# Optimization experiments

Measured on AMD Instinct MI355X. Metric: run time of the kernel, lower is better.

The kernel has to match this reference:

```python
import jax, jax.numpy as jnp
import numpy as np


def _ln(x, w, b, eps=1e-5):
    m = x.mean(-1, keepdims=True)
    v = jnp.mean((x - m) ** 2, axis=-1, keepdims=True)
    return (x - m) * jax.lax.rsqrt(v + eps) * w + b


def _to_seq(xc, g):
    # xc: [B,Di,H,W] -> [B,L,Di]; g0: row-major fwd, g1: row-major rev,
    # g2: col-major fwd, g3: col-major rev (CrossScan_1..4)
    if g >= 2:
        xc = xc.transpose(0, 1, 3, 2)
    s = xc.reshape(xc.shape[0], xc.shape[1], -1)
    if g % 2 == 1:
        s = jnp.flip(s, -1)
    return s.transpose(0, 2, 1)


def _from_seq(y, g, H, W):
    # y: [B,L,Di] -> [B,H,W,Di], inverse of _to_seq (CrossMerge_1..4)
    if g % 2 == 1:
        y = jnp.flip(y, 1)
    Bn, L, Di = y.shape
    if g >= 2:
        return y.reshape(Bn, W, H, Di).transpose(0, 2, 1, 3)
    return y.reshape(Bn, H, W, Di)


def _sscan(dA, dBx, Cm):
    # selective scan: h_t = dA_t*h + dBx_t ; y_t = <h_t, C_t>
    # dA,dBx: [B,L,Di,S], Cm: [B,L,S] -> y: [B,L,Di]
    def step(h, inp):
        a, bx, c = inp
        h = a * h + bx
        return h, jnp.einsum('bds,bs->bd', h, c)
    h0 = jnp.zeros(dA.shape[:1] + dA.shape[2:], dA.dtype)
    _, ys = jax.lax.scan(step, h0, (dA.transpose(1, 0, 2, 3), dBx.transpose(1, 0, 2, 3), Cm.transpose(1, 0, 2)))
    return ys.transpose(1, 0, 2)


def _ss2d(xc, g, H, W, ipw, ipb, cw, cb, xpw, dtw, dtb, A_log, Ds, onw, onb, opw, opb):
    R = dtw.shape[-1]
    S = A_log.shape[-1]
    xz = xc @ ipw.T + ipb                      # [B,H,W,2*Di]
    Di = xz.shape[-1] // 2
    xi, z = xz[..., :Di], xz[..., Di:]
    xi = xi.transpose(0, 3, 1, 2)              # [B,Di,H,W]
    xi = jax.lax.conv_general_dilated(xi, cw, (1, 1), [(1, 1), (1, 1)],
                                      dimension_numbers=('NCHW', 'OIHW', 'NCHW'),
                                      feature_group_count=Di) + cb[None, :, None, None]
    xi = jax.nn.silu(xi)
    seq = _to_seq(xi, g)                       # [B,L,Di]
    xdbl = seq @ xpw.T                         # [B,L,R+2S]
    dtr, Bm, Cm = xdbl[..., :R], xdbl[..., R:R + S], xdbl[..., R + S:]
    dt = jax.nn.softplus(dtr @ dtw.T + dtb)    # [B,L,Di]
    A = -jnp.exp(A_log)                        # [Di,S]
    dA = jnp.exp(dt[..., None] * A)            # [B,L,Di,S]
    dBx = (dt * seq)[..., None] * Bm[:, :, None, :]
    y = _sscan(dA, dBx, Cm) + Ds * seq
    y = _from_seq(y, g, H, W)                  # [B,H,W,Di]
    y = _ln(y, onw, onb)
    y = y * jax.nn.silu(z)
    return y @ opw.T + opb


def setup_inputs() -> dict:
    Bn, Hh, Ww, C = 8, 96, 96, 256
    Di = C // 4
    S = 1
    R = max(1, (Di + 15) // 16)
    key = jax.random.key(0)
    ks = jax.random.split(key, 12)
    nrm = lambda k, sh, s: jax.random.normal(k, sh, jnp.float32) * s
    return {
        'x': nrm(ks[0], (Bn, Hh * Ww, C), 1.0),
        'norm_w': jnp.ones((C,), jnp.float32), 'norm_b': jnp.zeros((C,), jnp.float32),
        'fc_w': nrm(ks[1], (C, C), 0.02), 'fc_b': jnp.zeros((C,), jnp.float32),
        'conv1d_w': nrm(ks[2], (1, 1, 3), 0.3),
        'in_proj_w': nrm(ks[3], (4, 2 * Di, Di), 0.05), 'in_proj_b': jnp.zeros((4, 2 * Di), jnp.float32),
        'conv2d_w': nrm(ks[4], (4, Di, 1, 3, 3), 0.2), 'conv2d_b': jnp.zeros((4, Di), jnp.float32),
        'x_proj_w': nrm(ks[5], (4, R + 2 * S, Di), 0.05),
        'dt_w': nrm(ks[6], (4, Di, R), 0.1), 'dt_b': nrm(ks[7], (4, Di), 0.1),
        'A_log': nrm(ks[8], (4, Di, S), 0.1),
        'Ds': jnp.ones((4, Di), jnp.float32),
        'out_norm_w': jnp.ones((4, Di), jnp.float32), 'out_norm_b': jnp.zeros((4, Di), jnp.float32),
        'out_proj_w': nrm(ks[9], (4, Di, Di), 0.05), 'out_proj_b': jnp.zeros((4, Di), jnp.float32),
        'proj_w': nrm(ks[10], (C, C), 0.02), 'proj_b': jnp.zeros((C,), jnp.float32),
        'skip_scale': jnp.ones((1,), jnp.float32),
        'H': Hh, 'W': Ww,
    }


def reference(x, norm_w, norm_b, fc_w, fc_b, conv1d_w, in_proj_w, in_proj_b, conv2d_w, conv2d_b,
              x_proj_w, dt_w, dt_b, A_log, Ds, out_norm_w, out_norm_b, out_proj_w, out_proj_b,
              proj_w, proj_b, skip_scale, H, W):
    B, N, C = x.shape
    xn = _ln(x, norm_w, norm_b)
    z_avg = xn.mean(1)                         # [B,C] (permute(0,2,1).mean(2))
    yg = jax.lax.conv_general_dilated(z_avg[:, None, :], conv1d_w, (1,), [(1, 1)],
                                      dimension_numbers=('NCH', 'OIH', 'NCH'))[:, 0, :]
    gate = jax.nn.sigmoid(z_avg @ fc_w.T + fc_b + yg)   # fc_out_2 [B,C]
    xg = xn.reshape(B, H, W, C)
    Dg = C // 4
    outs = [_ss2d(xg[..., g * Dg:(g + 1) * Dg], g, H, W,
                  in_proj_w[g], in_proj_b[g], conv2d_w[g], conv2d_b[g], x_proj_w[g],
                  dt_w[g], dt_b[g], A_log[g], Ds[g], out_norm_w[g], out_norm_b[g],
                  out_proj_w[g], out_proj_b[g]) for g in range(4)]
    xm = jnp.concatenate(outs, -1) * skip_scale * xg
    xm = xm.reshape(B, N, C) * gate[:, None, :]
    xm = _ln(xm, norm_w, norm_b)
    return xm @ proj_w.T + proj_b
```

## Files before the change

### kernel.cpp

```cpp
#include <hip/hip_runtime.h>
#include <math.h>

#define HH 96
#define WWI 96
#define NN 9216
#define CC 256
#define LL 9216
#define CHK 96
#define NCH 96
#define BB 8
#define BN (BB*NN)

__device__ __forceinline__ float softplusf(float x){
    float e = expf(-fabsf(x));
    return fmaxf(x, 0.f) + log1pf(e);
}
__device__ __forceinline__ float sigmf(float x){ return 1.f / (1.f + expf(-x)); }

__device__ __forceinline__ float wredsum(float v){
    #pragma unroll
    for(int o = 32; o > 0; o >>= 1) v += __shfl_xor(v, o, 64);
    return v;
}

__device__ __forceinline__ void wredsum2(float& s, float& q){
    #pragma unroll
    for(int o = 32; o > 0; o >>= 1){
        s += __shfl_xor(s, o, 64);
        q += __shfl_xor(q, o, 64);
    }
}

__device__ __forceinline__ void chunk_walk(int g, int chunk, int& base, int& step){
    if(g == 0){ base = chunk * 96;        step = 1;   }
    else if(g == 1){ base = 9215 - chunk * 96; step = -1; }
    else if(g == 2){ base = chunk;        step = 96;  }
    else { base = 9215 - chunk;           step = -96; }
}

__global__ __launch_bounds__(256) void k_stats(const float* __restrict__ x,
                                               float* __restrict__ mrs){
    int wid = threadIdx.x >> 6, lane = threadIdx.x & 63;
    size_t row = (size_t)blockIdx.x * 4 + wid;
    float4 v = ((const float4*)(x + row * CC))[lane];
    float s = wredsum(v.x + v.y + v.z + v.w);
    float q = wredsum(v.x*v.x + v.y*v.y + v.z*v.z + v.w*v.w);
    float m = s * (1.f/256.f);
    float var = q * (1.f/256.f) - m*m;
    float rs = rsqrtf(fmaxf(var, 0.f) + 1e-5f);
    if(lane == 0){ mrs[2*row] = m; mrs[2*row+1] = rs; }
}

__global__ __launch_bounds__(256) void k_prew(const float* __restrict__ pw,
        const float* __restrict__ nw, const float* __restrict__ nb,
        const float* __restrict__ pb, float* __restrict__ Wn,
        float* __restrict__ wsum, float* __restrict__ cvec){
    int o = threadIdx.x;
    float ws = 0.f, cc = 0.f;
    for(int k = 0; k < 256; k++){
        float w = pw[(size_t)o * 256 + k];
        float wn = w * nw[k];
        Wn[(size_t)o * 256 + k] = wn;
        ws += wn; cc += w * nb[k];
    }
    wsum[o] = ws; cvec[o] = cc + pb[o];
}

__global__ __launch_bounds__(256) void k_zavg(const float* __restrict__ x,
        const float* __restrict__ mrs, const float* __restrict__ nw,
        const float* __restrict__ nb, float* __restrict__ zpart){
    int c = threadIdx.x, b = blockIdx.y, t0 = blockIdx.x * 256;
    float nwv = nw[c], nbv = nb[c];
    float s = 0.f;
    for(int i = 0; i < 256; i++){
        size_t r = (size_t)b * NN + t0 + i;
        s += (x[r * CC + c] - mrs[2*r]) * mrs[2*r+1] * nwv + nbv;
    }
    zpart[((size_t)b * 36 + blockIdx.x) * CC + c] = s;
}

__global__ __launch_bounds__(256) void k_gate(const float* __restrict__ zpart,
        const float* __restrict__ fcw, const float* __restrict__ fcb,
        const float* __restrict__ w1d, float* __restrict__ gate){
    __shared__ float za[CC];
    int c = threadIdx.x, b = blockIdx.x;
    float s = 0.f;
    for(int t = 0; t < 36; t++) s += zpart[((size_t)b * 36 + t) * CC + c];
    za[c] = s * (1.f/(float)NN);
    __syncthreads();
    float zm1 = (c > 0)     ? za[c-1] : 0.f;
    float zp1 = (c < CC-1)  ? za[c+1] : 0.f;
    float acc = fcb[c] + w1d[0]*zm1 + w1d[1]*za[c] + w1d[2]*zp1;
    const float* wr = fcw + (size_t)c * CC;
    for(int k = 0; k < CC; k++) acc += za[k] * wr[k];
    gate[b * CC + c] = sigmf(acc);
}

__global__ __launch_bounds__(256) void k_inproj(const float* __restrict__ x,
        const float* __restrict__ mrs, const float* __restrict__ nw,
        const float* __restrict__ nb, const float* __restrict__ ipw,
        const float* __restrict__ ipb, float* __restrict__ xib,
        float* __restrict__ zbuf){
    int tile = blockIdx.x, b = blockIdx.y, g = blockIdx.z;
    int n0 = tile * 128;
    __shared__ float xs[128 * 64];
    int tid = threadIdx.x;
    for(int idx = tid; idx < 2048; idx += 256){
        int p = idx >> 4, k4 = (idx & 15) * 4;
        size_t r = (size_t)b * NN + n0 + p;
        float4 v = *(const float4*)(x + r * CC + g*64 + k4);
        float m = mrs[2*r], rs = mrs[2*r+1];
        float4 w4 = *(const float4*)(nw + g*64 + k4);
        float4 b4 = *(const float4*)(nb + g*64 + k4);
        float4 o;
        o.x = (v.x - m)*rs*w4.x + b4.x;
        o.y = (v.y - m)*rs*w4.y + b4.y;
        o.z = (v.z - m)*rs*w4.z + b4.z;
        o.w = (v.w - m)*rs*w4.w + b4.w;
        *(float4*)(xs + p*64 + k4) = o;
    }
    __syncthreads();
    int c = tid & 63, ph = tid >> 6;
    float wx[64], wz[64];
    {
        const float* wrx = ipw + ((size_t)(g*128 + c)) * 64;
        const float* wrz = ipw + ((size_t)(g*128 + 64 + c)) * 64;
        #pragma unroll
        for(int k = 0; k < 64; k++){ wx[k] = wrx[k]; wz[k] = wrz[k]; }
    }
    float bx = ipb[g*128 + c], bz = ipb[g*128 + 64 + c];
    size_t obase = ((size_t)(b*4 + g)) * NN + n0;
    for(int p = ph*32; p < ph*32 + 32; p++){
        const float4* xp = (const float4*)(xs + p*64);
        float a0 = 0.f, a1 = 0.f, z0 = 0.f, z1 = 0.f;
        #pragma unroll
        for(int k4 = 0; k4 < 16; k4 += 2){
            float4 u = xp[k4], v = xp[k4+1];
            a0 += u.x*wx[4*k4+0]; a1 += u.y*wx[4*k4+1];
            a0 += u.z*wx[4*k4+2]; a1 += u.w*wx[4*k4+3];
            z0 += u.x*wz[4*k4+0]; z1 += u.y*wz[4*k4+1];
            z0 += u.z*wz[4*k4+2]; z1 += u.w*wz[4*k4+3];
            a0 += v.x*wx[4*k4+4]; a1 += v.y*wx[4*k4+5];
            a0 += v.z*wx[4*k4+6]; a1 += v.w*wx[4*k4+7];
            z0 += v.x*wz[4*k4+4]; z1 += v.y*wz[4*k4+5];
            z0 += v.z*wz[4*k4+6]; z1 += v.w*wz[4*k4+7];
        }
        float xv = bx + a0 + a1;
        float zv = bz + z0 + z1;
        xib[(obase + p)*64 + c] = xv;
        zbuf[(obase + p)*64 + c] = zv * sigmf(zv);
    }
}

__global__ __launch_bounds__(256) void k_conv(const float* __restrict__ xib,
        const float* __restrict__ cw, const float* __restrict__ cb,
        float* __restrict__ out){
    int tile = blockIdx.x, b = blockIdx.y, g = blockIdx.z;
    int h0 = (tile/12)*8, w0 = (tile%12)*8;
    __shared__ float xs[100*64];
    int tid = threadIdx.x;
    size_t ibase = ((size_t)(b*4+g)) * NN;
    for(int i = tid; i < 6400; i += 256){
        int p = i >> 6, k = i & 63;
        int ph = h0 + p/10 - 1, pw = w0 + p%10 - 1;
        float v = 0.f;
        if(ph >= 0 && ph < HH && pw >= 0 && pw < WWI)
            v = xib[(ibase + (size_t)(ph*WWI + pw))*64 + k];
        xs[i] = v;
    }
    __syncthreads();
    int c = tid & 63, q = tid >> 6;
    float wk[9];
    const float* wp = cw + ((size_t)(g*64 + c))*9;
    #pragma unroll
    for(int j = 0; j < 9; j++) wk[j] = wp[j];
    float bias2 = cb[g*64 + c];
    for(int pi = q*16; pi < q*16+16; pi++){
        int py = pi >> 3, px = pi & 7;
        float acc = bias2;
        #pragma unroll
        for(int dy = 0; dy < 3; dy++)
            #pragma unroll
            for(int dx = 0; dx < 3; dx++)
                acc += xs[((py+dy)*10 + px+dx)*64 + c] * wk[dy*3+dx];
        float sv = acc * sigmf(acc);
        size_t r = (size_t)b*NN + (h0+py)*WWI + (w0+px);
        out[r*CC + g*64 + c] = sv;
    }
}

template<int ZPRE>
__global__ __launch_bounds__(256) void k_ipconv(const float* __restrict__ x,
        const float* __restrict__ mrs, const float* __restrict__ nw,
        const float* __restrict__ nb, const float* __restrict__ ipw,
        const float* __restrict__ ipb, const float* __restrict__ cw,
        const float* __restrict__ cb, float* __restrict__ out,
        float* __restrict__ zbuf){
    int tile = blockIdx.x, b = blockIdx.y, g = blockIdx.z;
    int h0 = (tile / 12) * 8, w0 = (tile % 12) * 8;
    __shared__ float xs[100 * 64];
    __shared__ float xi[100 * 64];
    int tid = threadIdx.x;
    for(int i = tid; i < 6400; i += 256){
        int p = i >> 6, k = i & 63;
        int ph = h0 + p / 10 - 1, pw = w0 + p % 10 - 1;
        float v = 0.f;
        if(ph >= 0 && ph < HH && pw >= 0 && pw < WWI){
            size_t r = (size_t)b * NN + ph * WWI + pw;
            v = (x[r * CC + g*64 + k] - mrs[2*r]) * mrs[2*r+1]
                * nw[g*64 + k] + nb[g*64 + k];
        }
        xs[i] = v;
    }
    __syncthreads();
    int c = tid & 63, q = tid >> 6;
    {
        float wv[64];
        const float* wr = ipw + ((size_t)(g * 128 + c)) * 64;
        #pragma unroll
        for(int k = 0; k < 64; k++) wv[k] = wr[k];
        float bias = ipb[g * 128 + c];
        for(int p = q * 25; p < q * 25 + 25; p++){
            int ph = h0 + p / 10 - 1, pw = w0 + p % 10 - 1;
            bool valid = (ph >= 0 && ph < HH && pw >= 0 && pw < WWI);
            float acc = bias;
            const float* xp = &xs[p * 64];
            #pragma unroll
            for(int k = 0; k < 64; k++) acc += xp[k] * wv[k];
            xi[p * 64 + c] = valid ? acc : 0.f;
        }
    }
    __syncthreads();
    float wk[9];
    const float* wp = cw + ((size_t)(g * 64 + c)) * 9;
    #pragma unroll
    for(int j = 0; j < 9; j++) wk[j] = wp[j];
    float bias2 = cb[g * 64 + c];
    for(int pi = q * 16; pi < q * 16 + 16; pi++){
        int py = pi >> 3, px = pi & 7;
        float acc = bias2;
        #pragma unroll
        for(int dy = 0; dy < 3; dy++)
            #pragma unroll
            for(int dx = 0; dx < 3; dx++)
                acc += xi[((py + dy) * 10 + px + dx) * 64 + c] * wk[dy*3 + dx];
        float sv = acc * sigmf(acc);
        size_t r = (size_t)b * NN + (h0 + py) * WWI + (w0 + px);
        out[r * CC + g*64 + c] = sv;
    }
    if(ZPRE){
        float wzv[64];
        const float* wr = ipw + ((size_t)(g * 128 + 64 + c)) * 64;
        #pragma unroll
        for(int k = 0; k < 64; k++) wzv[k] = wr[k];
        float zbv = ipb[g * 128 + 64 + c];
        size_t zb0 = ((size_t)(b * 4 + g)) * NN;
        for(int p16 = 0; p16 < 16; p16++){
            int p = q * 16 + p16;
            int py = p >> 3, px = p & 7;
            const float* xp = &xs[((py + 1) * 10 + (px + 1)) * 64];
            float acc = zbv;
            #pragma unroll
            for(int k = 0; k < 64; k++) acc += xp[k] * wzv[k];
            zbuf[(zb0 + (size_t)((h0 + py) * WWI + (w0 + px))) * 64 + c]
                = acc * sigmf(acc);
        }
    }
}

__global__ __launch_bounds__(64) void k_scan1(const float* __restrict__ out,
        const float* __restrict__ xpw, const float* __restrict__ dtw,
        const float* __restrict__ dtb, const float* __restrict__ alog,
        float* __restrict__ ap_out, float* __restrict__ h_out){
    int chunk = blockIdx.x, gb = blockIdx.y;
    int g = gb >> 3, b = gb & 7, d = threadIdx.x;
    __shared__ float s_seq[CHK * 65];
    __shared__ float s_xd[CHK * 6];
    __shared__ float s_w[6 * 64];
    int base, step; chunk_walk(g, chunk, base, step);
    const float* xg = out + (size_t)b * NN * CC + g * 64;
    for(int j = 0; j < CHK; j++)
        s_seq[j * 65 + d] = xg[(size_t)(base + j * step) * CC + d];
    for(int i = d; i < 384; i += 64) s_w[i] = xpw[g * 384 + i];
    __syncthreads();
    for(int idx = d; idx < CHK*6; idx += 64){
        int l = idx / 6, j = idx % 6;
        float acc = 0.f;
        const float* sr = &s_seq[l * 65];
        const float* wr = &s_w[j * 64];
        #pragma unroll
        for(int k = 0; k < 64; k++) acc += sr[k] * wr[k];
        s_xd[idx] = acc;
    }
    __syncthreads();
    int gd = g * 64 + d;
    float Av = -expf(alog[gd]);
    float db = dtb[gd];
    float w0 = dtw[gd*4], w1 = dtw[gd*4+1], w2 = dtw[gd*4+2], w3 = dtw[gd*4+3];
    float h = 0.f, apd = 1.f;
    #pragma unroll 4
    for(int l = 0; l < CHK; l++){
        const float* xd = &s_xd[l * 6];
        float xv = s_seq[l*65 + d];
        float dt = softplusf(xd[0]*w0 + xd[1]*w1 + xd[2]*w2 + xd[3]*w3 + db);
        float a = expf(dt * Av);
        h = a*h + dt*xv*xd[4];
        apd *= a;
    }
    int ob = (gb * NCH + chunk) * 64 + d;
    ap_out[ob] = apd; h_out[ob] = h;
}

__global__ __launch_bounds__(256) void k_scan2(const float* __restrict__ ap,
        const float* __restrict__ he, float* __restrict__ hinit){
    int idx = blockIdx.x * 256 + threadIdx.x;
    int gb = idx >> 6, d = idx & 63;
    float h = 0.f;
    for(int c = 0; c < NCH; c++){
        int o = (gb * NCH + c) * 64 + d;
        hinit[o] = h;
        h = ap[o]*h + he[o];
    }
}

template<int ZPRE>
__global__ __launch_bounds__(64) void k_scan3(float* __restrict__ out,
        const float* __restrict__ x, const float* __restrict__ mrs,
        const float* __restrict__ nw, const float* __restrict__ nb,
        const float* __restrict__ ipw, const float* __restrict__ ipb,
        const float* __restrict__ xpw, const float* __restrict__ dtw,
        const float* __restrict__ dtb, const float* __restrict__ alog,
        const float* __restrict__ Dsp, const float* __restrict__ onw,
        const float* __restrict__ onb, const float* __restrict__ hinit,
        const float* __restrict__ zbuf){
    int chunk = blockIdx.x, gb = blockIdx.y;
    int g = gb >> 3, b = gb & 7, d = threadIdx.x;
    __shared__ float s_seq[CHK * 65];
    __shared__ float s_xd[CHK * 6];
    __shared__ float s_w[6 * 64];
    __shared__ float xnt[(ZPRE ? 1 : CHK) * 65];
    int base, step; chunk_walk(g, chunk, base, step);
    float* xg = out + (size_t)b * NN * CC + g * 64;
    for(int j = 0; j < CHK; j++)
        s_seq[j * 65 + d] = xg[(size_t)(base + j * step) * CC + d];
    if(!ZPRE){
        float nwv = nw[g*64 + d], nbv = nb[g*64 + d];
        for(int j = 0; j < CHK; j++){
            int n = base + j * step;
            size_t r = (size_t)b * NN + n;
            xnt[j * 65 + d] = (x[r * CC + g*64 + d] - mrs[2*r]) * mrs[2*r+1] * nwv + nbv;
        }
    }
    for(int i = d; i < 384; i += 64) s_w[i] = xpw[g * 384 + i];
    __syncthreads();
    for(int idx = d; idx < CHK*6; idx += 64){
        int l = idx / 6, j = idx % 6;
        float acc = 0.f;
        const float* sr = &s_seq[l * 65];
        const float* wr = &s_w[j * 64];
        #pragma unroll
        for(int k = 0; k < 64; k++) acc += sr[k] * wr[k];
        s_xd[idx] = acc;
    }
    __syncthreads();
    int gd = g * 64 + d;
    float Av = -expf(alog[gd]);
    float db = dtb[gd];
    float Dv = Dsp[gd];
    float w0 = dtw[gd*4], w1 = dtw[gd*4+1], w2 = dtw[gd*4+2], w3 = dtw[gd*4+3];
    float h = hinit[(gb * NCH + chunk) * 64 + d];
    #pragma unroll 4
    for(int l = 0; l < CHK; l++){
        const float* xd = &s_xd[l * 6];
        float xv = s_seq[l*65 + d];
        float dt = softplusf(xd[0]*w0 + xd[1]*w1 + xd[2]*w2 + xd[3]*w3 + db);
        float a = expf(dt * Av);
        h = a*h + dt*xv*xd[4];
        s_seq[l*65 + d] = h * xd[5] + Dv * xv;
    }
    float wON = onw[gd], bON = onb[gd];
    float wz[ZPRE ? 1 : 64];
    float zb = 0.f;
    if(!ZPRE){
        const float* wr = ipw + ((size_t)(g * 128 + 64 + d)) * 64;
        #pragma unroll
        for(int k = 0; k < 64; k++) wz[k] = wr[k];
        zb = ipb[g * 128 + 64 + d];
    }
    const float* zp = zbuf + (((size_t)(b * 4 + g)) * NN) * 64 + d;
    #pragma unroll 4
    for(int l = 0; l < CHK; l++){
        float y = s_seq[l*65 + d];
        float s = y, q = y * y;
        wredsum2(s, q);
        float m = s * (1.f/64.f);
        float var = q * (1.f/64.f) - m*m;
        float rs = rsqrtf(fmaxf(var, 0.f) + 1e-5f);
        float lny = (y - m) * rs * wON + bON;
        int n = base + l * step;
        float zs;
        if(ZPRE){
            zs = zp[(size_t)n * 64];
        } else {
            float z = zb;
            const float* xp = &xnt[l * 65];
            #pragma unroll
            for(int k = 0; k < 64; k++) z += xp[k] * wz[k];
            zs = z * sigmf(z);
        }
        xg[(size_t)n * CC + d] = lny * zs;
    }
}

__global__ __launch_bounds__(64) void k_out2(float* __restrict__ out,
        const float* __restrict__ x, const float* __restrict__ mrs,
        const float* __restrict__ nw, const float* __restrict__ nb,
        const float* __restrict__ opw, const float* __restrict__ opb,
        const float* __restrict__ gate, const float* __restrict__ skip){
    int tile = blockIdx.x, b = blockIdx.y, g = blockIdx.z;
    int n0 = tile * 64, t = threadIdx.x;
    __shared__ float ly[64 * 65];
    __shared__ float xnt[64 * 65];
    float* xg = out + (size_t)b * NN * CC + g * 64;
    float nwv = nw[g*64 + t], nbv = nb[g*64 + t];
    for(int p = 0; p < 64; p++){
        size_t r = (size_t)b * NN + n0 + p;
        ly[p * 65 + t] = xg[(size_t)(n0 + p) * CC + t];
        xnt[p * 65 + t] = (x[r * CC + g*64 + t] - mrs[2*r]) * mrs[2*r+1] * nwv + nbv;
    }
    __syncthreads();
    float wv[64];
    const float* wr = opw + ((size_t)(g * 64 + t)) * 64;
    #pragma unroll
    for(int k = 0; k < 64; k++) wv[k] = wr[k];
    float bias = opb[g * 64 + t];
    float gv = gate[b * CC + g*64 + t];
    float sk = skip[0];
    for(int p = 0; p < 64; p++){
        float acc = bias;
        const float* yp = &ly[p * 65];
        #pragma unroll
        for(int k = 0; k < 64; k++) acc += yp[k] * wv[k];
        xg[(size_t)(n0 + p) * CC + t] = acc * sk * xnt[p * 65 + t] * gv;
    }
}

__global__ __launch_bounds__(256) void k_out3(const float* __restrict__ yin,
        const float* __restrict__ x, const float* __restrict__ mrs,
        const float* __restrict__ nw, const float* __restrict__ nb,
        const float* __restrict__ opw, const float* __restrict__ opb,
        const float* __restrict__ gate, const float* __restrict__ skip,
        float* __restrict__ zo, float* __restrict__ mrs2){
    __shared__ float ps[16 * 4], pq[16 * 4];
    int o = threadIdx.x;
    int g = o >> 6, c = o & 63;
    int r0 = blockIdx.x * 16;
    int b  = r0 / NN;
    int n0 = r0 - b * NN;
    float wv[64];
    {
        const float4* wr = (const float4*)(opw + ((size_t)(g*64 + c)) * 64);
        #pragma unroll
        for(int j = 0; j < 16; j++){
            float4 t4 = wr[j];
            wv[4*j+0] = t4.x; wv[4*j+1] = t4.y;
            wv[4*j+2] = t4.z; wv[4*j+3] = t4.w;
        }
    }
    float acc[16];
    const float* ab = yin + ((size_t)b * NN + n0) * CC + g * 64;
    #pragma unroll 4
    for(int r = 0; r < 16; r++){
        const float4* ar = (const float4*)(ab + (size_t)r * CC);
        float s0 = 0.f, s1 = 0.f;
        #pragma unroll
        for(int j = 0; j < 8; j++){
            float4 u = ar[j], v = ar[j + 8];
            s0 += u.x*wv[4*j+0]  + u.y*wv[4*j+1]  + u.z*wv[4*j+2]  + u.w*wv[4*j+3];
            s1 += v.x*wv[32+4*j] + v.y*wv[33+4*j] + v.z*wv[34+4*j] + v.w*wv[35+4*j];
        }
        acc[r] = s0 + s1;
    }
    float bias = opb[g*64 + c];
    float gv = gate[b * CC + g*64 + c];
    float sk = skip[0];
    float nwv = nw[g*64 + c], nbv = nb[g*64 + c];
    size_t zbase = ((size_t)(b*4 + g)) * NN + n0;
    #pragma unroll
    for(int r = 0; r < 16; r++){
        size_t row = (size_t)r0 + r;
        float xv = x[row * CC + g*64 + c];
        float xn = (xv - mrs[2*row]) * mrs[2*row+1] * nwv + nbv;
        float res = (acc[r] + bias) * sk * xn * gv;
        acc[r] = res;
        zo[(zbase + r) * 64 + c] = res;
    }
    #pragma unroll
    for(int r = 0; r < 16; r++){
        float s = acc[r], q = acc[r] * acc[r];
        wredsum2(s, q);
        if(c == 0){ ps[r*4 + g] = s; pq[r*4 + g] = q; }
    }
    __syncthreads();
    if(o < 16){
        float ss = ps[o*4] + ps[o*4+1] + ps[o*4+2] + ps[o*4+3];
        float qq = pq[o*4] + pq[o*4+1] + pq[o*4+2] + pq[o*4+3];
        float m = ss * (1.f/256.f);
        float var = qq * (1.f/256.f) - m*m;
        mrs2[2*((size_t)r0 + o)]     = m;
        mrs2[2*((size_t)r0 + o) + 1] = rsqrtf(fmaxf(var, 0.f) + 1e-5f);
    }
}

__global__ __launch_bounds__(256) void k_final(float* __restrict__ out,
        const float* __restrict__ nw, const float* __restrict__ nb,
        const float* __restrict__ pw, const float* __restrict__ pb){
    __shared__ float A[16 * 256];
    __shared__ float ps[256], pq[256];
    __shared__ float mrow[16], rrow[16];
    int n0 = blockIdx.x * 16;
    for(int i = threadIdx.x; i < 4096; i += 256)
        A[i] = out[(size_t)n0 * CC + i];
    __syncthreads();
    {
        int r = threadIdx.x >> 4, t16 = threadIdx.x & 15;
        float s = 0.f, q = 0.f;
        for(int j = 0; j < 16; j++){
            float v = A[r*256 + t16*16 + j];
            s += v; q += v*v;
        }
        ps[threadIdx.x] = s; pq[threadIdx.x] = q;
    }
    __syncthreads();
    if(threadIdx.x < 16){
        float ss = 0.f, qq = 0.f;
        for(int j = 0; j < 16; j++){ ss += ps[threadIdx.x*16 + j]; qq += pq[threadIdx.x*16 + j]; }
        float m = ss * (1.f/256.f);
        float var = qq * (1.f/256.f) - m*m;
        mrow[threadIdx.x] = m;
        rrow[threadIdx.x] = rsqrtf(fmaxf(var, 0.f) + 1e-5f);
    }
    __syncthreads();
    for(int i = threadIdx.x; i < 4096; i += 256){
        int r = i >> 8, c = i & 255;
        A[i] = (A[i] - mrow[r]) * rrow[r] * nw[c] + nb[c];
    }
    __syncthreads();
    int o = threadIdx.x;
    float acc[16];
    #pragma unroll
    for(int p = 0; p < 16; p++) acc[p] = 0.f;
    for(int kt = 0; kt < 4; kt++){
        float wv[64];
        const float4* wr = (const float4*)(pw + (size_t)o * CC + kt * 64);
        #pragma unroll
        for(int j = 0; j < 16; j++){
            float4 tq = wr[j];
            wv[4*j+0] = tq.x; wv[4*j+1] = tq.y;
            wv[4*j+2] = tq.z; wv[4*j+3] = tq.w;
        }
        #pragma unroll
        for(int p = 0; p < 16; p++){
            const float* ar = &A[p*256 + kt*64];
            float a = 0.f;
            #pragma unroll
            for(int k = 0; k < 64; k++) a += ar[k] * wv[k];
            acc[p] += a;
        }
    }
    float pbv = pb[o];
    #pragma unroll
    for(int p = 0; p < 16; p++)
        out[(size_t)(n0 + p) * CC + o] = acc[p] + pbv;
}

__global__ __launch_bounds__(256) void k_final2(const float* __restrict__ y,
        const float* __restrict__ mrs2, const float* __restrict__ Wn,
        const float* __restrict__ wsum, const float* __restrict__ cvec,
        float* __restrict__ out){
    int o = threadIdx.x;
    int r0 = blockIdx.x * 16;
    int b  = r0 / NN;
    int n0 = r0 - b * NN;
    float acc[16];
    #pragma unroll
    for(int r = 0; r < 16; r++) acc[r] = 0.f;
    for(int kt = 0; kt < 4; kt++){
        float wv[64];
        const float4* wr = (const float4*)(Wn + (size_t)o * 256 + kt * 64);
        #pragma unroll
        for(int j = 0; j < 16; j++){
            float4 t4 = wr[j];
            wv[4*j+0] = t4.x; wv[4*j+1] = t4.y;
            wv[4*j+2] = t4.z; wv[4*j+3] = t4.w;
        }
        const float* ab = y + ((size_t)(b*4 + kt)*NN + n0) * 64;
        #pragma unroll 4
        for(int r = 0; r < 16; r++){
            const float* ar = ab + (size_t)r * 64;
            float s0 = 0.f, s1 = 0.f;
            #pragma unroll
            for(int j = 0; j < 32; j++){
                s0 += ar[j]      * wv[j];
                s1 += ar[j + 32] * wv[j + 32];
            }
            acc[r] += s0 + s1;
        }
    }
    float wso = wsum[o], co = cvec[o];
    #pragma unroll
    for(int r = 0; r < 16; r++){
        float m  = mrs2[2*(size_t)(r0 + r)];
        float rs = mrs2[2*(size_t)(r0 + r) + 1];
        out[(size_t)(r0 + r) * CC + o] = rs * acc[r] - m * rs * wso + co;
    }
}

extern "C" void kernel_launch(void* const* d_in, const int* in_sizes, int n_in,
                              void* d_out, int out_size, void* d_ws, size_t ws_size,
                              hipStream_t stream){
    const float* x    = (const float*)d_in[0];
    const float* nw   = (const float*)d_in[1];
    const float* nb   = (const float*)d_in[2];
    const float* fcw  = (const float*)d_in[3];
    const float* fcb  = (const float*)d_in[4];
    const float* w1d  = (const float*)d_in[5];
    const float* ipw  = (const float*)d_in[6];
    const float* ipb  = (const float*)d_in[7];
    const float* cw   = (const float*)d_in[8];
    const float* cb   = (const float*)d_in[9];
    const float* xpw  = (const float*)d_in[10];
    const float* dtw  = (const float*)d_in[11];
    const float* dtb  = (const float*)d_in[12];
    const float* alog = (const float*)d_in[13];
    const float* Dsp  = (const float*)d_in[14];
    const float* onw  = (const float*)d_in[15];
    const float* onb  = (const float*)d_in[16];
    const float* opw  = (const float*)d_in[17];
    const float* opb  = (const float*)d_in[18];
    const float* pw   = (const float*)d_in[19];
    const float* pb   = (const float*)d_in[20];
    const float* skip = (const float*)d_in[21];

    char* base = (char*)d_ws;
    float* mrs  = (float*)base;
    float* gate = (float*)(base +  589824ull);
    float* ap   = (float*)(base +  598016ull);
    float* he   = (float*)(base + 1384448ull);
    float* hi   = (float*)(base + 2170880ull);
    float* zbuf = (float*)(base + 2957312ull);
    float* mrs2 = (float*)(base + 78454784ull);
    float* Wn   = (float*)(base + 79044608ull);
    float* wsum = (float*)(base + 79306752ull);
    float* cvec = (float*)(base + 79307776ull);
    float* xib  = (float*)(base + 79308800ull);
    float* zpart = ap;
    float* out  = (float*)d_out;
    (void)in_sizes; (void)n_in; (void)out_size;

    const size_t T1 = 78454784ull;
    const size_t T2 = 79308800ull;
    const size_t T3 = 154806272ull;
    bool usez    = ws_size >= T1;
    bool usef2   = ws_size >= T2;
    bool usesplit= ws_size >= T3;

    if(usef2)
        k_prew<<<1, 256, 0, stream>>>(pw, nw, nb, pb, Wn, wsum, cvec);
    k_stats <<<18432, 256, 0, stream>>>(x, mrs);
    k_zavg  <<<dim3(36, 8), 256, 0, stream>>>(x, mrs, nw, nb, zpart);
    k_gate  <<<8, 256, 0, stream>>>(zpart, fcw, fcb, w1d, gate);
    if(usesplit){
        k_inproj<<<dim3(72, 8, 4), 256, 0, stream>>>(x, mrs, nw, nb, ipw, ipb,
                                                     xib, zbuf);
        k_conv  <<<dim3(144, 8, 4), 256, 0, stream>>>(xib, cw, cb, out);
    } else if(usez){
        k_ipconv<1><<<dim3(144, 8, 4), 256, 0, stream>>>(x, mrs, nw, nb, ipw, ipb,
                                                         cw, cb, out, zbuf);
    } else {
        k_ipconv<0><<<dim3(144, 8, 4), 256, 0, stream>>>(x, mrs, nw, nb, ipw, ipb,
                                                         cw, cb, out, zbuf);
    }
    k_scan1 <<<dim3(96, 32), 64, 0, stream>>>(out, xpw, dtw, dtb, alog, ap, he);
    k_scan2 <<<8, 256, 0, stream>>>(ap, he, hi);
    if(usez){
        k_scan3<1><<<dim3(96, 32), 64, 0, stream>>>(out, x, mrs, nw, nb, ipw, ipb,
                                                    xpw, dtw, dtb, alog, Dsp, onw,
                                                    onb, hi, zbuf);
    } else {
        k_scan3<0><<<dim3(96, 32), 64, 0, stream>>>(out, x, mrs, nw, nb, ipw, ipb,
                                                    xpw, dtw, dtb, alog, Dsp, onw,
                                                    onb, hi, zbuf);
    }
    if(usef2){
        k_out3  <<<4608, 256, 0, stream>>>(out, x, mrs, nw, nb, opw, opb,
                                           gate, skip, zbuf, mrs2);
        k_final2<<<4608, 256, 0, stream>>>(zbuf, mrs2, Wn, wsum, cvec, out);
    } else {
        k_out2  <<<dim3(144, 8, 4), 64, 0, stream>>>(out, x, mrs, nw, nb, opw, opb,
                                                     gate, skip);
        k_final <<<4608, 256, 0, stream>>>(out, nw, nb, pw, pb);
    }
}
```

Before: 1.226 ms.

## Fold LayerNorm into in_proj weights and use register-resident weight GEMV kernel

Adds a precompute kernel that folds the LayerNorm scale and bias into the per-group in_proj weights, plus per-output weight sums and bias constants. The in-projection then works on raw x, applying the per-row mean and rstd afterwards. A new kernel keeps one output channel's 64 weights in registers and streams 16 rows of x per block, replacing the shared-memory tiled version. The new path runs only when the workspace is large enough for the extra buffers. In exchange it uses high register pressure and redundant global reads of x across threads.

```diff
diff --git a/kernel.cpp b/kernel.cpp
--- a/kernel.cpp
+++ b/kernel.cpp
@@ -66,6 +66,23 @@
     wsum[o] = ws; cvec[o] = cc + pb[o];
 }
 
+__global__ __launch_bounds__(128) void k_prewip(const float* __restrict__ ipw,
+        const float* __restrict__ nw, const float* __restrict__ nb,
+        const float* __restrict__ ipb, float* __restrict__ Wip,
+        float* __restrict__ wsip, float* __restrict__ cvip){
+    int g = blockIdx.x, o = threadIdx.x;
+    const float* wr = ipw + ((size_t)(g*128 + o)) * 64;
+    float ws = 0.f, cc = 0.f;
+    for(int k = 0; k < 64; k++){
+        float w = wr[k];
+        float wn = w * nw[g*64 + k];
+        Wip[((size_t)(g*128 + o))*64 + k] = wn;
+        ws += wn; cc += w * nb[g*64 + k];
+    }
+    wsip[g*128 + o] = ws;
+    cvip[g*128 + o] = cc + ipb[g*128 + o];
+}
+
 __global__ __launch_bounds__(256) void k_zavg(const float* __restrict__ x,
         const float* __restrict__ mrs, const float* __restrict__ nw,
         const float* __restrict__ nb, float* __restrict__ zpart){
@@ -94,6 +111,56 @@
     const float* wr = fcw + (size_t)c * CC;
     for(int k = 0; k < CC; k++) acc += za[k] * wr[k];
     gate[b * CC + c] = sigmf(acc);
+}
+
+__global__ __launch_bounds__(256) void k_inproj2(const float* __restrict__ x,
+        const float* __restrict__ mrs, const float* __restrict__ Wip,
+        const float* __restrict__ wsip, const float* __restrict__ cvip,
+        float* __restrict__ xib, float* __restrict__ zbuf){
+    int t = threadIdx.x;
+    int g = blockIdx.y * 2 + (t >> 7);
+    int h = (t >> 6) & 1;
+    int c = t & 63;
+    int r0 = blockIdx.x * 16;
+    int b  = r0 / NN;
+    int n0 = r0 - b * NN;
+    int oc = g*128 + h*64 + c;
+    float wv[64];
+    {
+        const float4* wr = (const float4*)(Wip + (size_t)oc * 64);
+        #pragma unroll
+        for(int j = 0; j < 16; j++){
+            float4 t4 = wr[j];
+            wv[4*j+0] = t4.x; wv[4*j+1] = t4.y;
+            wv[4*j+2] = t4.z; wv[4*j+3] = t4.w;
+        }
+    }
+    float acc[16];
+    const float* ab = x + (size_t)r0 * CC + g * 64;
+    #pragma unroll 4
+    for(int r = 0; r < 16; r++){
+        const float4* ar = (const float4*)(ab + (size_t)r * CC);
+        float s0 = 0.f, s1 = 0.f;
+        #pragma unroll
+        for(int j = 0; j < 8; j++){
+            float4 u = ar[j], v = ar[j + 8];
+            s0 += u.x*wv[4*j+0]  + u.y*wv[4*j+1]  + u.z*wv[4*j+2]  + u.w*wv[4*j+3];
+            s1 += v.x*wv[32+4*j] + v.y*wv[33+4*j] + v.z*wv[34+4*j] + v.w*wv[35+4*j];
+        }
+        acc[r] = s0 + s1;
+    }
+    float ws = wsip[oc], cv = cvip[oc];
+    size_t obase = ((size_t)(b*4 + g)) * NN + n0;
+    #pragma unroll
+    for(int r = 0; r < 16; r++){
+        size_t row = (size_t)r0 + r;
+        float m = mrs[2*row], rs = mrs[2*row+1];
+        float v = rs * acc[r] - m * rs * ws + cv;
+        if(h == 0)
+            xib[(obase + r)*64 + c] = v;
+        else
+            zbuf[(obase + r)*64 + c] = v * sigmf(v);
+    }
 }
 
 __global__ __launch_bounds__(256) void k_inproj(const float* __restrict__ x,
@@ -654,6 +721,9 @@
     float* wsum = (float*)(base + 79306752ull);
     float* cvec = (float*)(base + 79307776ull);
     float* xib  = (float*)(base + 79308800ull);
+    float* Wip  = (float*)(base + 154806272ull);
+    float* wsip = (float*)(base + 154937344ull);
+    float* cvip = (float*)(base + 154939392ull);
     float* zpart = ap;
     float* out  = (float*)d_out;
     (void)in_sizes; (void)n_in; (void)out_size;
@@ -661,16 +731,24 @@
     const size_t T1 = 78454784ull;
     const size_t T2 = 79308800ull;
     const size_t T3 = 154806272ull;
+    const size_t T4 = 154941440ull;
     bool usez    = ws_size >= T1;
     bool usef2   = ws_size >= T2;
     bool usesplit= ws_size >= T3;
+    bool useip2  = ws_size >= T4;
 
     if(usef2)
         k_prew<<<1, 256, 0, stream>>>(pw, nw, nb, pb, Wn, wsum, cvec);
+    if(useip2)
+        k_prewip<<<4, 128, 0, stream>>>(ipw, nw, nb, ipb, Wip, wsip, cvip);
     k_stats <<<18432, 256, 0, stream>>>(x, mrs);
     k_zavg  <<<dim3(36, 8), 256, 0, stream>>>(x, mrs, nw, nb, zpart);
     k_gate  <<<8, 256, 0, stream>>>(zpart, fcw, fcb, w1d, gate);
-    if(usesplit){
+    if(useip2){
+        k_inproj2<<<dim3(4608, 2), 256, 0, stream>>>(x, mrs, Wip, wsip, cvip,
+                                                     xib, zbuf);
+        k_conv  <<<dim3(144, 8, 4), 256, 0, stream>>>(xib, cw, cb, out);
+    } else if(usesplit){
         k_inproj<<<dim3(72, 8, 4), 256, 0, stream>>>(x, mrs, nw, nb, ipw, ipb,
                                                      xib, zbuf);
         k_conv  <<<dim3(144, 8, 4), 256, 0, stream>>>(xib, cw, cb, out);
```

Measured after the change: 1.348 ms. 1.1x slower.
